# Performance work log

Hardware: AMD Instinct MI355X
Metric: run time of the kernel (lower is better)

Reference implementation:

```python
import jax, jax.numpy as jnp
import numpy as np

DIM = 512
NUM_HEADS = 16
HEAD_DIM = DIM // NUM_HEADS
HIDDEN = int(DIM * 4.0)
EPS = 1e-5


def layer_norm(x, gamma, beta):
    mu = jnp.mean(x, axis=-1, keepdims=True)
    var = jnp.mean(jnp.square(x - mu), axis=-1, keepdims=True)
    return (x - mu) * jax.lax.rsqrt(var + EPS) * gamma + beta


def setup_inputs() -> dict:
    key = jax.random.key(0)
    ks = jax.random.split(key, 8)
    B, L, C = 32, 3136, DIM
    x = jax.random.normal(ks[0], (B, L, C), dtype=jnp.float32)
    norm1_g = jnp.ones((C,), jnp.float32)
    norm1_b = jnp.zeros((C,), jnp.float32)
    # spatial (per-head) mixing weight: (num_heads, head_dim, head_dim)
    w_spatial = jax.random.normal(ks[1], (NUM_HEADS, HEAD_DIM, HEAD_DIM), jnp.float32) * (1.0 / np.sqrt(HEAD_DIM))
    norm2_g = jnp.ones((C,), jnp.float32)
    norm2_b = jnp.zeros((C,), jnp.float32)
    w1 = jax.random.normal(ks[2], (C, HIDDEN), jnp.float32) * (1.0 / np.sqrt(C))
    b1 = jnp.zeros((HIDDEN,), jnp.float32)
    w2 = jax.random.normal(ks[3], (HIDDEN, C), jnp.float32) * (1.0 / np.sqrt(HIDDEN))
    b2 = jnp.zeros((C,), jnp.float32)
    return {"x": x, "norm1_g": norm1_g, "norm1_b": norm1_b, "w_spatial": w_spatial,
            "norm2_g": norm2_g, "norm2_b": norm2_b, "w1": w1, "b1": b1, "w2": w2, "b2": b2}


def reference(x, norm1_g, norm1_b, w_spatial, norm2_g, norm2_b, w1, b1, w2, b2):
    B, L, C = x.shape
    shortcut = x
    h = layer_norm(x, norm1_g, norm1_b)
    # window partition -> per-head channel-sub-dim linear (shared across windows/positions)
    # mathematically equivalent to applying the per-head matmul at every token
    h = h.reshape(B, L, NUM_HEADS, HEAD_DIM)
    h = jnp.einsum('blhd,hde->blhe', h, w_spatial)
    h = h.reshape(B, L, C)
    x = shortcut + h
    # channel MLP: Linear -> GELU(tanh) -> Linear
    y = layer_norm(x, norm2_g, norm2_b)
    y = jax.nn.gelu(y @ w1 + b1, approximate=True)
    y = y @ w2 + b2
    return x + y
```

## Files before the change

### kernel.cpp

```cpp
#include <hip/hip_runtime.h>
#include <hip/hip_bf16.h>


typedef __bf16 bf16x8 __attribute__((ext_vector_type(8)));
typedef float f32x16 __attribute__((ext_vector_type(16)));

constexpr int CDIM = 512;
constexpr int HID = 2048;
constexpr int MROWS = 32 * 3136;
constexpr float LN_EPS = 1e-5f;

static __device__ __forceinline__ float gelu_tanh(float x) {
  const float u = 0.7978845608028654f * fmaf(0.044715f * x * x, x, x);
  const float e = __expf(2.0f * u);
  return 0.5f * x * (2.0f - 2.0f / (e + 1.0f));
}

static __device__ __forceinline__ void load_lds16(const void* g, void* l) {
  __builtin_amdgcn_global_load_lds((__attribute__((address_space(1))) void*)g,
                                   (__attribute__((address_space(3))) void*)l,
                                   16, 0, 0);
}

template <int KD, int ND>
__global__ __launch_bounds__(256) void cvt_pack32(
    const float* __restrict__ src, __hip_bfloat16* __restrict__ dst) {
  constexpr int NKT2 = KD / 16;
  const int o = blockIdx.x * 256 + threadIdx.x;
  const int l = o & 63;
  const int gt = o >> 6;
  const int t = gt & (NKT2 - 1), g = gt / NKT2;
  const int n = g * 32 + (l & 31);
  const int k0 = t * 16 + (l >> 5) * 8;
  __hip_bfloat16 v[8];
#pragma unroll
  for (int j = 0; j < 8; ++j)
    v[j] = __float2bfloat16(src[(size_t)(k0 + j) * ND + n]);
  *(uint4*)(dst + (size_t)o * 8) = *(const uint4*)v;
}

__global__ __launch_bounds__(256) void fused_pre(
    const float* __restrict__ x, const float* __restrict__ g1,
    const float* __restrict__ b1, const float* __restrict__ wsp,
    const float* __restrict__ g2, const float* __restrict__ b2,
    float* __restrict__ x2out, __hip_bfloat16* __restrict__ yout) {
  __shared__ float lnbuf[4][CDIM];
  __shared__ float red[4][4][2];

  const int t = threadIdx.x;
  const int lane = t & 63;
  const int w = t >> 6;
  const int c0 = 2 * t;
  const int hd = c0 >> 5, e0 = c0 & 31;

  float wc0[32], wc1[32];
#pragma unroll
  for (int d = 0; d < 32; ++d) {
    const float2 wv = *(const float2*)&wsp[(hd * 32 + d) * 32 + e0];
    wc0[d] = wv.x;
    wc1[d] = wv.y;
  }
  const float2 g1v = *(const float2*)&g1[c0];
  const float2 b1v = *(const float2*)&b1[c0];
  const float2 g2v = *(const float2*)&g2[c0];
  const float2 b2v = *(const float2*)&b2[c0];

  for (int rq = blockIdx.x; rq < MROWS / 4; rq += gridDim.x) {
    const size_t r0 = (size_t)rq * 4;
    float2 xv[4];
#pragma unroll
    for (int r = 0; r < 4; ++r)
      xv[r] = *(const float2*)&x[(r0 + r) * CDIM + c0];

    float s[4], q[4];
#pragma unroll
    for (int r = 0; r < 4; ++r) {
      s[r] = xv[r].x + xv[r].y;
      q[r] = xv[r].x * xv[r].x + xv[r].y * xv[r].y;
    }
#pragma unroll
    for (int off = 32; off; off >>= 1)
#pragma unroll
      for (int r = 0; r < 4; ++r) {
        s[r] += __shfl_down(s[r], off);
        q[r] += __shfl_down(q[r], off);
      }
    if (lane == 0)
#pragma unroll
      for (int r = 0; r < 4; ++r) {
        red[w][r][0] = s[r];
        red[w][r][1] = q[r];
      }
    __syncthreads();
    float mu[4], rs[4];
#pragma unroll
    for (int r = 0; r < 4; ++r) {
      s[r] = red[0][r][0] + red[1][r][0] + red[2][r][0] + red[3][r][0];
      q[r] = red[0][r][1] + red[1][r][1] + red[2][r][1] + red[3][r][1];
      mu[r] = s[r] * (1.0f / CDIM);
      rs[r] = rsqrtf(q[r] * (1.0f / CDIM) - mu[r] * mu[r] + LN_EPS);
      lnbuf[r][c0] = (xv[r].x - mu[r]) * rs[r] * g1v.x + b1v.x;
      lnbuf[r][c0 + 1] = (xv[r].y - mu[r]) * rs[r] * g1v.y + b1v.y;
    }
    __syncthreads();

    float h[4][2] = {};
#pragma unroll
    for (int d = 0; d < 32; ++d) {
#pragma unroll
      for (int r = 0; r < 4; ++r) {
        const float lv = lnbuf[r][hd * 32 + d];
        h[r][0] = fmaf(lv, wc0[d], h[r][0]);
        h[r][1] = fmaf(lv, wc1[d], h[r][1]);
      }
    }
    float a[4][2];
#pragma unroll
    for (int r = 0; r < 4; ++r) {
      a[r][0] = xv[r].x + h[r][0];
      a[r][1] = xv[r].y + h[r][1];
      float2 av;
      av.x = a[r][0];
      av.y = a[r][1];
      *(float2*)&x2out[(r0 + r) * CDIM + c0] = av;
      s[r] = a[r][0] + a[r][1];
      q[r] = a[r][0] * a[r][0] + a[r][1] * a[r][1];
    }
#pragma unroll
    for (int off = 32; off; off >>= 1)
#pragma unroll
      for (int r = 0; r < 4; ++r) {
        s[r] += __shfl_down(s[r], off);
        q[r] += __shfl_down(q[r], off);
      }
    if (lane == 0)
#pragma unroll
      for (int r = 0; r < 4; ++r) {
        red[w][r][0] = s[r];
        red[w][r][1] = q[r];
      }
    __syncthreads();
#pragma unroll
    for (int r = 0; r < 4; ++r) {
      s[r] = red[0][r][0] + red[1][r][0] + red[2][r][0] + red[3][r][0];
      q[r] = red[0][r][1] + red[1][r][1] + red[2][r][1] + red[3][r][1];
      mu[r] = s[r] * (1.0f / CDIM);
      rs[r] = rsqrtf(q[r] * (1.0f / CDIM) - mu[r] * mu[r] + LN_EPS);
      __hip_bfloat162 yv;
      yv.x = __float2bfloat16((a[r][0] - mu[r]) * rs[r] * g2v.x + b2v.x);
      yv.y = __float2bfloat16((a[r][1] - mu[r]) * rs[r] * g2v.y + b2v.y);
      *(__hip_bfloat162*)&yout[(r0 + r) * CDIM + c0] = yv;
    }
    __syncthreads();
  }
}

template <int K, int N, bool GELU>
__global__ __launch_bounds__(256, 3) void gemm32(
    const __hip_bfloat16* __restrict__ A, const char* __restrict__ Bp,
    const float* __restrict__ bias, __hip_bfloat16* __restrict__ zout,
    float* __restrict__ fout) {
  constexpr int NT = N / 128;
  constexpr int NKT2 = K / 16;
  constexpr int NST = K / 32;
  __shared__ __attribute__((aligned(16))) char smem[32768];

  const int tid = threadIdx.x;
  const int lane = tid & 63;
  const int w = tid >> 6;
  const int wr = w >> 1, wc = w & 1;

  const int cpx = gridDim.x >> 3;
  const int bid = (blockIdx.x & 7) * cpx + (blockIdx.x >> 3);
  const int tm = bid / NT, tn = bid - tm * NT;
  const size_t am0 = (size_t)tm * 128;
  const int bn0 = tn * 128;

  const int r0 = tid >> 2, q0 = tid & 3;
  const __hip_bfloat16* aP0 = A + (am0 + r0) * K + q0 * 8;
  const __hip_bfloat16* aP1 = aP0 + (size_t)64 * K;
  const int wb = w * 1024;

  const int arow = (lane & 31);
  const int akb = (lane >> 5) * 16;
  const int abase = (wr * 64 + arow) * 64 + akb;

  const char* bBase =
      Bp + ((size_t)(tn * 4 + wc * 2) * NKT2) * 1024 + lane * 16;

#define STAGE_A(so, kt)                                       \
  do {                                                        \
    load_lds16(aP0 + (kt) * 32, smem + (so) + wb);            \
    load_lds16(aP1 + (kt) * 32, smem + (so) + 4096 + wb);     \
  } while (0)

  f32x16 acc[2][2] = {};
  bf16x8 bf[2][2], bfn[2][2], af[2][2];

  STAGE_A(0, 0);
#pragma unroll
  for (int ni = 0; ni < 2; ++ni)
#pragma unroll
    for (int kh = 0; kh < 2; ++kh)
      bf[ni][kh] = *(const bf16x8*)(bBase + ((size_t)ni * NKT2 + kh) * 1024);
  __syncthreads();

  for (int t = 0; t < NST; ++t) {
    const int d = (t & 1) * 8192, dn = 8192 - d;
    if (t + 1 < NST) {
      STAGE_A(dn, t + 1);
#pragma unroll
      for (int ni = 0; ni < 2; ++ni)
#pragma unroll
        for (int kh = 0; kh < 2; ++kh)
          bfn[ni][kh] = *(const bf16x8*)(bBase +
                                         ((size_t)ni * NKT2 + 2 * (t + 1) + kh) *
                                             1024);
    }

#pragma unroll
    for (int mi = 0; mi < 2; ++mi)
#pragma unroll
      for (int kh = 0; kh < 2; ++kh)
        af[mi][kh] =
            *(const bf16x8*)(smem + d + abase + mi * 2048 + kh * 32);
#pragma unroll
    for (int kh = 0; kh < 2; ++kh)
#pragma unroll
      for (int mi = 0; mi < 2; ++mi)
#pragma unroll
        for (int ni = 0; ni < 2; ++ni)
          acc[mi][ni] = __builtin_amdgcn_mfma_f32_32x32x16_bf16(
              af[mi][kh], bf[ni][kh], acc[mi][ni], 0, 0, 0);
    if (t + 1 < NST) {
#pragma unroll
      for (int ni = 0; ni < 2; ++ni)
#pragma unroll
        for (int kh = 0; kh < 2; ++kh) bf[ni][kh] = bfn[ni][kh];
    }
    __syncthreads();
  }
#undef STAGE_A

  const int ccol = lane & 31;
  const int rbase = 4 * (lane >> 5);
  char* smb = smem;

  if constexpr (GELU) {
    __hip_bfloat16* ot = (__hip_bfloat16*)smb;
#pragma unroll
    for (int ni = 0; ni < 2; ++ni) {
      const int col = wc * 64 + ni * 32 + ccol;
      const float bv = bias[bn0 + col];
#pragma unroll
      for (int mi = 0; mi < 2; ++mi)
#pragma unroll
        for (int r = 0; r < 16; ++r) {
          const int row = wr * 64 + mi * 32 + (r & 3) + 8 * (r >> 2) + rbase;
          ot[row * 128 + col] =
              __float2bfloat16(gelu_tanh(acc[mi][ni][r] + bv));
        }
    }
    __syncthreads();
#pragma unroll
    for (int it = 0; it < 8; ++it) {
      const int seg = it * 256 + tid;
      const int row = seg >> 4, cs = seg & 15;
      const uint4 v = *(const uint4*)(smb + seg * 16);
      *(uint4*)&zout[(am0 + row) * N + bn0 + cs * 8] = v;
    }
  } else {
    float* ot = (float*)smb;
#pragma unroll
    for (int p = 0; p < 2; ++p) {
      if (p) __syncthreads();
      if (wr == p) {
#pragma unroll
        for (int ni = 0; ni < 2; ++ni) {
          const int col = wc * 64 + ni * 32 + ccol;
          const float bv = bias[bn0 + col];
#pragma unroll
          for (int mi = 0; mi < 2; ++mi)
#pragma unroll
            for (int r = 0; r < 16; ++r) {
              const int rl = mi * 32 + (r & 3) + 8 * (r >> 2) + rbase;
              ot[rl * 128 + col] = acc[mi][ni][r] + bv;
            }
        }
      }
      __syncthreads();
#pragma unroll
      for (int it = 0; it < 8; ++it) {
        const int seg = it * 256 + tid;
        const int row = seg >> 5, cs = seg & 31;
        const float4 lv = *(const float4*)(smb + seg * 16);
        float* gp = &fout[(am0 + p * 64 + row) * N + bn0 + cs * 4];
        float4 o = *(const float4*)gp;
        o.x += lv.x;
        o.y += lv.y;
        o.z += lv.z;
        o.w += lv.w;
        *(float4*)gp = o;
      }
    }
  }
}

extern "C" void kernel_launch(void* const* d_in, const int* in_sizes, int n_in,
                              void* d_out, int out_size, void* d_ws,
                              size_t ws_size, hipStream_t stream) {
  const float* x = (const float*)d_in[0];
  const float* n1g = (const float*)d_in[1];
  const float* n1b = (const float*)d_in[2];
  const float* wsp = (const float*)d_in[3];
  const float* n2g = (const float*)d_in[4];
  const float* n2b = (const float*)d_in[5];
  const float* w1 = (const float*)d_in[6];
  const float* b1 = (const float*)d_in[7];
  const float* w2 = (const float*)d_in[8];
  const float* b2 = (const float*)d_in[9];
  float* out = (float*)d_out;

  __hip_bfloat16* ybuf = (__hip_bfloat16*)d_ws;
  __hip_bfloat16* zbuf = ybuf + (size_t)MROWS * CDIM;
  __hip_bfloat16* w1p = zbuf + (size_t)MROWS * HID;
  __hip_bfloat16* w2p = w1p + (size_t)CDIM * HID;

  cvt_pack32<CDIM, HID><<<512, 256, 0, stream>>>(w1, w1p);
  cvt_pack32<HID, CDIM><<<512, 256, 0, stream>>>(w2, w2p);
  fused_pre<<<2048, 256, 0, stream>>>(x, n1g, n1b, wsp, n2g, n2b, out, ybuf);
  gemm32<CDIM, HID, true><<<(MROWS / 128) * (HID / 128), 256, 0, stream>>>(
      ybuf, (const char*)w1p, b1, zbuf, nullptr);
  gemm32<HID, CDIM, false><<<(MROWS / 128) * (CDIM / 128), 256, 0, stream>>>(
      zbuf, (const char*)w2p, b2, nullptr, out);
}
```

Before: 866.2 us.

## Store activations in MFMA-fragment-packed layout for contiguous A-tile loads

The LayerNorm output and the GELU intermediate are now written in a blocked layout of 32-row by 16-column tiles, each 1 KB, matching the MFMA A-operand fragment order. The GEMM stages A with contiguous 16-byte-per-lane loads and reads LDS fragments linearly, with no strided row addressing. This is meant to cut global-load transactions and LDS bank conflicts on the A path. In exchange, the producer stores in fused_pre and the GELU epilogue become more scattered, which may cost some write efficiency.

```diff
diff --git a/kernel.cpp b/kernel.cpp
--- a/kernel.cpp
+++ b/kernel.cpp
@@ -52,6 +52,7 @@
   const int w = t >> 6;
   const int c0 = 2 * t;
   const int hd = c0 >> 5, e0 = c0 & 31;
+  const int ypc32 = (c0 >> 4) * 512 + ((c0 >> 3) & 1) * 256 + (c0 & 7);
 
   float wc0[32], wc1[32];
 #pragma unroll
@@ -149,18 +150,20 @@
       __hip_bfloat162 yv;
       yv.x = __float2bfloat16((a[r][0] - mu[r]) * rs[r] * g2v.x + b2v.x);
       yv.y = __float2bfloat16((a[r][1] - mu[r]) * rs[r] * g2v.y + b2v.y);
-      *(__hip_bfloat162*)&yout[(r0 + r) * CDIM + c0] = yv;
+      const size_t rr = r0 + r;
+      *(__hip_bfloat162*)&yout[(rr >> 5) * 16384 + (rr & 31) * 8 + ypc32] = yv;
     }
     __syncthreads();
   }
 }
 
 template <int K, int N, bool GELU>
-__global__ __launch_bounds__(256, 3) void gemm32(
-    const __hip_bfloat16* __restrict__ A, const char* __restrict__ Bp,
-    const float* __restrict__ bias, __hip_bfloat16* __restrict__ zout,
+__global__ __launch_bounds__(256, 3) void gemm32p(
+    const char* __restrict__ Ap, const char* __restrict__ Bp,
+    const float* __restrict__ bias, char* __restrict__ zp,
     float* __restrict__ fout) {
   constexpr int NT = N / 128;
+  constexpr int NKT2A = K / 16;
   constexpr int NKT2 = K / 16;
   constexpr int NST = K / 32;
   __shared__ __attribute__((aligned(16))) char smem[32768];
@@ -176,22 +179,20 @@
   const size_t am0 = (size_t)tm * 128;
   const int bn0 = tn * 128;
 
-  const int r0 = tid >> 2, q0 = tid & 3;
-  const __hip_bfloat16* aP0 = A + (am0 + r0) * K + q0 * 8;
-  const __hip_bfloat16* aP1 = aP0 + (size_t)64 * K;
-  const int wb = w * 1024;
-
-  const int arow = (lane & 31);
-  const int akb = (lane >> 5) * 16;
-  const int abase = (wr * 64 + arow) * 64 + akb;
+  const size_t aBlk0 = ((size_t)(tm * 4 + (tid >> 7)) * NKT2A + ((tid >> 6) & 1));
+  const size_t aBlk1 = aBlk0 + (size_t)2 * NKT2A;
+  const char* aP0 = Ap + aBlk0 * 1024 + lane * 16;
+  const char* aP1 = Ap + aBlk1 * 1024 + lane * 16;
+  const int ldsA0 = (tid >> 6) * 1024;
+  const int ldsA1 = 4096 + (tid >> 6) * 1024;
 
   const char* bBase =
       Bp + ((size_t)(tn * 4 + wc * 2) * NKT2) * 1024 + lane * 16;
 
-#define STAGE_A(so, kt)                                       \
-  do {                                                        \
-    load_lds16(aP0 + (kt) * 32, smem + (so) + wb);            \
-    load_lds16(aP1 + (kt) * 32, smem + (so) + 4096 + wb);     \
+#define STAGE_A(so, kt)                                   \
+  do {                                                    \
+    load_lds16(aP0 + (size_t)(kt) * 2048, smem + (so) + ldsA0); \
+    load_lds16(aP1 + (size_t)(kt) * 2048, smem + (so) + ldsA1); \
   } while (0)
 
   f32x16 acc[2][2] = {};
@@ -213,17 +214,17 @@
       for (int ni = 0; ni < 2; ++ni)
 #pragma unroll
         for (int kh = 0; kh < 2; ++kh)
-          bfn[ni][kh] = *(const bf16x8*)(bBase +
-                                         ((size_t)ni * NKT2 + 2 * (t + 1) + kh) *
-                                             1024);
+          bfn[ni][kh] =
+              *(const bf16x8*)(bBase +
+                               ((size_t)ni * NKT2 + 2 * (t + 1) + kh) * 1024);
     }
 
 #pragma unroll
     for (int mi = 0; mi < 2; ++mi)
 #pragma unroll
       for (int kh = 0; kh < 2; ++kh)
-        af[mi][kh] =
-            *(const bf16x8*)(smem + d + abase + mi * 2048 + kh * 32);
+        af[mi][kh] = *(const bf16x8*)(smem + d + ((wr * 2 + mi) * 2 + kh) * 1024 +
+                                      lane * 16);
 #pragma unroll
     for (int kh = 0; kh < 2; ++kh)
 #pragma unroll
@@ -247,17 +248,17 @@
   char* smb = smem;
 
   if constexpr (GELU) {
-    __hip_bfloat16* ot = (__hip_bfloat16*)smb;
 #pragma unroll
     for (int ni = 0; ni < 2; ++ni) {
       const int col = wc * 64 + ni * 32 + ccol;
       const float bv = bias[bn0 + col];
+      const int cpart = (col >> 4) * 1024 + ((col >> 3) & 1) * 512 + (col & 7) * 2;
 #pragma unroll
       for (int mi = 0; mi < 2; ++mi)
 #pragma unroll
         for (int r = 0; r < 16; ++r) {
           const int row = wr * 64 + mi * 32 + (r & 3) + 8 * (r >> 2) + rbase;
-          ot[row * 128 + col] =
+          *(__hip_bfloat16*)(smb + (row >> 5) * 8192 + (row & 31) * 16 + cpart) =
               __float2bfloat16(gelu_tanh(acc[mi][ni][r] + bv));
         }
     }
@@ -265,9 +266,10 @@
 #pragma unroll
     for (int it = 0; it < 8; ++it) {
       const int seg = it * 256 + tid;
-      const int row = seg >> 4, cs = seg & 15;
-      const uint4 v = *(const uint4*)(smb + seg * 16);
-      *(uint4*)&zout[(am0 + row) * N + bn0 + cs * 8] = v;
+      const int blk = seg >> 6, l = seg & 63;
+      const size_t gb =
+          ((size_t)(am0 >> 5) + (blk >> 3)) * (N / 16) + (bn0 >> 4) + (blk & 7);
+      *(uint4*)(zp + gb * 1024 + l * 16) = *(const uint4*)(smb + seg * 16);
     }
   } else {
     float* ot = (float*)smb;
@@ -329,8 +331,8 @@
   cvt_pack32<CDIM, HID><<<512, 256, 0, stream>>>(w1, w1p);
   cvt_pack32<HID, CDIM><<<512, 256, 0, stream>>>(w2, w2p);
   fused_pre<<<2048, 256, 0, stream>>>(x, n1g, n1b, wsp, n2g, n2b, out, ybuf);
-  gemm32<CDIM, HID, true><<<(MROWS / 128) * (HID / 128), 256, 0, stream>>>(
-      ybuf, (const char*)w1p, b1, zbuf, nullptr);
-  gemm32<HID, CDIM, false><<<(MROWS / 128) * (CDIM / 128), 256, 0, stream>>>(
-      zbuf, (const char*)w2p, b2, nullptr, out);
-}
+  gemm32p<CDIM, HID, true><<<(MROWS / 128) * (HID / 128), 256, 0, stream>>>(
+      (const char*)ybuf, (const char*)w1p, b1, (char*)zbuf, nullptr);
+  gemm32p<HID, CDIM, false><<<(MROWS / 128) * (CDIM / 128), 256, 0, stream>>>(
+      (const char*)zbuf, (const char*)w2p, b2, nullptr, out);
+}
```

Result: faster. 825.1 us (-4.7%).
